# Kernel tuning notes

Measured on AMD Instinct MI355X. Metric: run time of the kernel, lower is better.

The kernel has to match this reference:

```python
import jax, jax.numpy as jnp
import numpy as np

B, S, D = 8, 1024, 1024
H, DK = 16, 64  # heads, key_size (== head_size)
NEG = 1e12


def setup_inputs() -> dict:
    key = jax.random.key(0)
    ks = jax.random.split(key, 10)
    s = 1.0 / np.sqrt(D)
    return {
        "q": jax.random.normal(ks[0], (B, S, D), jnp.float32),
        "k": jax.random.normal(ks[1], (B, S, D), jnp.float32),
        "v": jax.random.normal(ks[2], (B, S, D), jnp.float32),
        "pos_bias": jax.random.normal(ks[3], (S, S, DK), jnp.float32) * 0.02,
        "Wq": jax.random.normal(ks[4], (D, H * DK), jnp.float32) * s,
        "Wk": jax.random.normal(ks[5], (D, H * DK), jnp.float32) * s,
        "Wv": jax.random.normal(ks[6], (D, H * DK), jnp.float32) * s,
        "Wo": jax.random.normal(ks[7], (H * DK, D), jnp.float32) * s,
        "bq": jnp.zeros((H * DK,), jnp.float32),
        "bk": jnp.zeros((H * DK,), jnp.float32),
        "bv": jnp.zeros((H * DK,), jnp.float32),
        "bo": jnp.zeros((D,), jnp.float32),
        "q_mask": jnp.ones((B, S), jnp.int32),
        "v_mask": jnp.ones((B, S), jnp.int32),
    }


def reference(q, k, v, pos_bias, Wq, Wk, Wv, Wo, bq, bk, bv, bo, q_mask, v_mask):
    qm = q_mask.astype(q.dtype)  # [B,Sq]
    vm = v_mask.astype(q.dtype)  # [B,Sk]
    # Projections (faithful quirk: K is projected from v, as in the source)
    qw = (q @ Wq + bq).reshape(B, S, H, DK)
    kw = (v @ Wk + bk).reshape(B, S, H, DK)
    vw = (v @ Wv + bv).reshape(B, S, H, DK)
    # scores + inline relative-position bias ('typial_relative' branch)
    a = jnp.einsum('bjhd,bkhd->bhjk', qw, kw)
    a = a + jnp.einsum('bjhd,jkd->bhjk', qw, pos_bias)
    a = a / jnp.sqrt(jnp.asarray(DK, a.dtype))
    # additive key mask, then softmax over keys
    a = a - (1.0 - vm)[:, None, None, :] * NEG
    a = jax.nn.softmax(a, axis=-1)
    o = jnp.einsum('bhjk,bkhd->bjhd', a, vw)  # [B,Sq,H,DK]
    o = o.reshape(B, S, H * DK) @ Wo + bo
    # multiplicative query mask on output
    o = o * qm[:, :, None]
    return o
```

## Files before the change

kernel.cpp:

```cpp
#include <hip/hip_runtime.h>

using short8 = __attribute__((ext_vector_type(8))) short;
using f32x4  = __attribute__((ext_vector_type(4))) float;
using f32x16 = __attribute__((ext_vector_type(16))) float;
using u16x4  = __attribute__((ext_vector_type(4))) unsigned short;
using fl4    = __attribute__((ext_vector_type(4))) float;

#define MFMA16(a, b, c) __builtin_amdgcn_mfma_f32_16x16x32_bf16((a), (b), (c), 0, 0, 0)
#define MFMA32(a, b, c) __builtin_amdgcn_mfma_f32_32x32x16_bf16((a), (b), (c), 0, 0, 0)

static __device__ __forceinline__ unsigned short f2bf(float f) {
  union { float f; unsigned u; } x; x.f = f;
  return (unsigned short)((x.u + 0x7FFFu + ((x.u >> 16) & 1u)) >> 16);
}
static __device__ __forceinline__ float bf2f(unsigned short s) {
  union { unsigned u; float f; } x; x.u = ((unsigned)s) << 16;
  return x.f;
}
static __device__ __forceinline__ float fexp2(float x) {
  float r; asm("v_exp_f32 %0, %1" : "=v"(r) : "v"(x)); return r;
}
static __device__ __forceinline__ unsigned pk2(float lo, float hi) {
  unsigned r; asm("v_cvt_pk_bf16_f32 %0, %1, %2" : "=v"(r) : "v"(lo), "v"(hi));
  return r;
}

static __device__ __forceinline__ void gload16(const void* g, void* l) {
  __builtin_amdgcn_global_load_lds((const __attribute__((address_space(1))) void*)g,
                                   (__attribute__((address_space(3))) void*)l, 16, 0, 0);
}

#define LOG2E 1.4426950408889634f

__global__ __launch_bounds__(256) void k_wconv4(
    const float* __restrict__ W0, const float* __restrict__ W1,
    const float* __restrict__ W2, const float* __restrict__ W3,
    unsigned short* __restrict__ Wt0, unsigned short* __restrict__ Wt1,
    unsigned short* __restrict__ Wt2, unsigned short* __restrict__ Wt3) {
  const float* W = (blockIdx.z == 0) ? W0 : (blockIdx.z == 1) ? W1
                   : (blockIdx.z == 2) ? W2 : W3;
  unsigned short* Wt = (blockIdx.z == 0) ? Wt0 : (blockIdx.z == 1) ? Wt1
                       : (blockIdx.z == 2) ? Wt2 : Wt3;
  __shared__ float tile[64][65];
  const int t = threadIdx.x;
  const int n0 = blockIdx.x * 64, k0 = blockIdx.y * 64;
#pragma unroll
  for (int p = 0; p < 4; ++p) {
    int row = p * 16 + (t >> 4);
    int c4 = (t & 15) * 4;
    fl4 val = *(const fl4*)&W[(size_t)(k0 + row) * 1024 + n0 + c4];
    tile[row][c4 + 0] = val[0];
    tile[row][c4 + 1] = val[1];
    tile[row][c4 + 2] = val[2];
    tile[row][c4 + 3] = val[3];
  }
  __syncthreads();
#pragma unroll
  for (int p = 0; p < 4; ++p) {
    int n = p * 16 + (t >> 4);
    int k4 = (t & 15) * 4;
    u16x4 u;
    u[0] = f2bf(tile[k4 + 0][n]);
    u[1] = f2bf(tile[k4 + 1][n]);
    u[2] = f2bf(tile[k4 + 2][n]);
    u[3] = f2bf(tile[k4 + 3][n]);
    *(u16x4*)&Wt[(size_t)(n0 + n) * 1024 + k0 + k4] = u;
  }
}

__global__ __launch_bounds__(256) void k_cvt(const float* __restrict__ a,
                                             const float* __restrict__ b,
                                             unsigned short* __restrict__ oa,
                                             unsigned short* __restrict__ ob) {
  const float* src = blockIdx.y ? b : a;
  unsigned short* dst = blockIdx.y ? ob : oa;
  size_t i = ((size_t)blockIdx.x * 256 + threadIdx.x) * 8;
  fl4 v0 = *(const fl4*)&src[i];
  fl4 v1 = *(const fl4*)&src[i + 4];
  u16x4 u0, u1;
  u0[0] = f2bf(v0[0]); u0[1] = f2bf(v0[1]); u0[2] = f2bf(v0[2]); u0[3] = f2bf(v0[3]);
  u1[0] = f2bf(v1[0]); u1[1] = f2bf(v1[1]); u1[2] = f2bf(v1[2]); u1[3] = f2bf(v1[3]);
  *(u16x4*)&dst[i] = u0;
  *(u16x4*)&dst[i + 4] = u1;
}

#define GEMM3_CORE(APTR, BPTR)                                                  \
  const int t = threadIdx.x, lane = t & 63, w = t >> 6;                         \
  const int g = lane >> 4, ln = lane & 15;                                      \
  const int wm = w >> 1, wn = w & 1;                                            \
  __shared__ unsigned short sh[24576];    \
  const int srow = lane >> 2;                                                   \
  const int sc = (lane & 3) ^ ((lane >> 3) & 3);                                \
  const int rsw = ((ln >> 1) & 3);                                              \
  f32x4 acc[4][4] = {};                                                         \
  _Pragma("unroll") for (int pre = 0; pre < 2; ++pre) {                         \
    _Pragma("unroll") for (int p = 0; p < 2; ++p) {                             \
      gload16(&APTR[(size_t)(m0 + p * 64 + w * 16 + srow) * 1024 + pre * 32 + sc * 8], \
              &sh[pre * 8192 + (p * 64 + w * 16) * 32]);                        \
      gload16(&BPTR[(size_t)(n0 + p * 64 + w * 16 + srow) * 1024 + pre * 32 + sc * 8], \
              &sh[pre * 8192 + 4096 + (p * 64 + w * 16) * 32]);                 \
    }                                                                           \
  }                                                                             \
  int cur = 0;                                                                  \
  for (int tt = 0; tt < 32; ++tt) {                                             \
    if (tt < 31) {                                                              \
      asm volatile("s_waitcnt vmcnt(4)" ::: "memory");                          \
    } else {                                                                    \
      asm volatile("s_waitcnt vmcnt(0)" ::: "memory");                          \
    }                                                                           \
    __builtin_amdgcn_sched_barrier(0);                                          \
    __builtin_amdgcn_s_barrier();                                               \
    __builtin_amdgcn_sched_barrier(0);                                          \
    if (tt < 30) {                                                              \
      int bb = cur + 2; if (bb >= 3) bb -= 3;                                   \
      int kk = (tt + 2) * 32;                                                   \
      _Pragma("unroll") for (int p = 0; p < 2; ++p) {                           \
        gload16(&APTR[(size_t)(m0 + p * 64 + w * 16 + srow) * 1024 + kk + sc * 8], \
                &sh[bb * 8192 + (p * 64 + w * 16) * 32]);                       \
        gload16(&BPTR[(size_t)(n0 + p * 64 + w * 16 + srow) * 1024 + kk + sc * 8], \
                &sh[bb * 8192 + 4096 + (p * 64 + w * 16) * 32]);                \
      }                                                                         \
    }                                                                           \
    const unsigned short* As = &sh[cur * 8192];                                 \
    const unsigned short* Bs = As + 4096;                                       \
    short8 af[4], bfr[4];                                                       \
    _Pragma("unroll") for (int fm = 0; fm < 4; ++fm)                            \
        af[fm] = *(const short8*)&As[(wm * 64 + fm * 16 + ln) * 32 + (g ^ rsw) * 8]; \
    _Pragma("unroll") for (int fn = 0; fn < 4; ++fn)                            \
        bfr[fn] = *(const short8*)&Bs[(wn * 64 + fn * 16 + ln) * 32 + (g ^ rsw) * 8]; \
    _Pragma("unroll") for (int fn = 0; fn < 4; ++fn) {                          \
      _Pragma("unroll") for (int fm = 0; fm < 4; ++fm)                          \
          acc[fm][fn] = MFMA16(af[fm], bfr[fn], acc[fm][fn]);                   \
    }                                                                           \
    cur = (cur == 2) ? 0 : cur + 1;                                             \
  }

__global__ __launch_bounds__(256) void k_proj3(
    const unsigned short* __restrict__ QB, const unsigned short* __restrict__ VB,
    const unsigned short* __restrict__ WtQ, const unsigned short* __restrict__ WtK,
    const unsigned short* __restrict__ WtV,
    const float* __restrict__ bq, const float* __restrict__ bk,
    const float* __restrict__ bv,
    unsigned short* __restrict__ QW, unsigned short* __restrict__ KW,
    unsigned short* __restrict__ VWT) {
  const int mode = blockIdx.z;
  const unsigned short* A8 = (mode == 0) ? QB : VB;
  const unsigned short* Wt = (mode == 0) ? WtQ : (mode == 1) ? WtK : WtV;
  const float* bias = (mode == 0) ? bq : (mode == 1) ? bk : bv;
  const int m0 = blockIdx.x * 128, n0 = blockIdx.y * 128;
  GEMM3_CORE(A8, Wt)
  __syncthreads();
  const float scale = (mode == 0) ? (0.125f * LOG2E) : 1.0f;
#pragma unroll
  for (int fn = 0; fn < 4; ++fn) {
    float bn = bias[n0 + wn * 64 + fn * 16 + ln];
#pragma unroll
    for (int fm = 0; fm < 4; ++fm) {
#pragma unroll
      for (int r = 0; r < 4; ++r) {
        float val = (acc[fm][fn][r] + bn) * scale;
        sh[(wm * 64 + fm * 16 + 4 * g + r) * 132 + wn * 64 + fn * 16 + ln] = f2bf(val);
      }
    }
  }
  __syncthreads();
  if (mode < 2) {
    unsigned short* OUT = (mode == 0) ? QW : KW;
#pragma unroll
    for (int p = 0; p < 16; ++p) {
      int row = p * 8 + (t >> 5), c4 = (t & 31) * 4;
      *(u16x4*)&OUT[(size_t)(m0 + row) * 1024 + n0 + c4] =
          *(const u16x4*)&sh[row * 132 + c4];
    }
  } else {
    const int b = m0 >> 10, s0 = m0 & 1023;
#pragma unroll
    for (int p = 0; p < 16; ++p) {
#pragma unroll
      for (int qh = 0; qh < 2; ++qh) {
        int hdl = p * 8 + (t >> 5);
        int sl = qh * 64 + (t & 31) * 2;
        unsigned lo = sh[sl * 132 + hdl];
        unsigned hi = sh[(sl + 1) * 132 + hdl];
        int hd = n0 + hdl;
        int h = hd >> 6, d = hd & 63;
        *(unsigned*)&VWT[((size_t)(b * 16 + h) * 64 + d) * 1024 + s0 + sl] =
            lo | (hi << 16);
      }
    }
  }
}

__global__ __launch_bounds__(256) void k_out3(
    const unsigned short* __restrict__ OB, const unsigned short* __restrict__ WtO,
    const float* __restrict__ bo, const int* __restrict__ qmask,
    float* __restrict__ out) {
  const int m0 = blockIdx.x * 128, n0 = blockIdx.y * 128;
  GEMM3_CORE(OB, WtO)
  float bn[4];
#pragma unroll
  for (int fn = 0; fn < 4; ++fn) bn[fn] = bo[n0 + wn * 64 + fn * 16 + ln];
#pragma unroll
  for (int fm = 0; fm < 4; ++fm) {
#pragma unroll
    for (int r = 0; r < 4; ++r) {
      int row = m0 + wm * 64 + fm * 16 + 4 * g + r;
      float qm = (float)qmask[row];
#pragma unroll
      for (int fn = 0; fn < 4; ++fn)
        out[(size_t)row * 1024 + n0 + wn * 64 + fn * 16 + ln] =
            (acc[fm][fn][r] + bn[fn]) * qm;
    }
  }
}

__global__ __launch_bounds__(256) void k_pbias(
    const unsigned short* __restrict__ QW, const float* __restrict__ pb,
    const int* __restrict__ vmask, unsigned short* __restrict__ CB, int jbase) {
  const int kt = blockIdx.y;
  const int jl = blockIdx.x;
  const int j = jbase + jl;
  const int t = threadIdx.x, lane = t & 63, w = t >> 6;
  const int g = lane >> 4, ln = lane & 15;
  const int wm = w >> 1, wn = w & 1;
  __shared__ unsigned short sm[18432];
  unsigned short* a_lds = sm;
  unsigned short* b_lds = sm + 9216;
#pragma unroll
  for (int p = 0; p < 8; ++p) {
    int i4 = p * 256 + t;
    int row = i4 >> 4, c4 = (i4 & 15) * 4;
    *(u16x4*)&a_lds[row * 72 + c4] =
        *(const u16x4*)&QW[((size_t)(row >> 4) * 1024 + j) * 1024 + (row & 15) * 64 + c4];
  }
#pragma unroll
  for (int p = 0; p < 8; ++p) {
    int i4 = p * 256 + t;
    int row = i4 >> 4, c4 = (i4 & 15) * 4;
    fl4 val = *(const fl4*)&pb[((size_t)j * 1024 + kt * 128 + row) * 64 + c4];
    u16x4 u;
    u[0] = f2bf(val[0]); u[1] = f2bf(val[1]);
    u[2] = f2bf(val[2]); u[3] = f2bf(val[3]);
    *(u16x4*)&b_lds[row * 72 + c4] = u;
  }
  __syncthreads();
  f32x4 acc[4][4] = {};
#pragma unroll
  for (int ks = 0; ks < 2; ++ks) {
    short8 af[4];
#pragma unroll
    for (int fm = 0; fm < 4; ++fm)
      af[fm] = *(const short8*)&a_lds[(wm * 64 + fm * 16 + ln) * 72 + ks * 32 + 8 * g];
#pragma unroll
    for (int fn = 0; fn < 4; ++fn) {
      short8 bfr = *(const short8*)&b_lds[(wn * 64 + fn * 16 + ln) * 72 + ks * 32 + 8 * g];
#pragma unroll
      for (int fm = 0; fm < 4; ++fm) acc[fm][fn] = MFMA16(af[fm], bfr, acc[fm][fn]);
    }
  }
  __syncthreads();
#pragma unroll
  for (int fn = 0; fn < 4; ++fn) {
    int kcol = kt * 128 + wn * 64 + fn * 16 + ln;
#pragma unroll
    for (int fm = 0; fm < 4; ++fm) {
      float off = vmask[(wm * 4 + fm) * 1024 + kcol] ? 0.f : (-1e12f * LOG2E);
#pragma unroll
      for (int r = 0; r < 4; ++r)
        sm[(wm * 64 + fm * 16 + 4 * g + r) * 132 + wn * 64 + fn * 16 + ln] =
            f2bf(acc[fm][fn][r] + off);
    }
  }
  __syncthreads();
#pragma unroll
  for (int p = 0; p < 16; ++p) {
    int row = p * 8 + (t >> 5), c4 = (t & 31) * 4;
    *(u16x4*)&CB[((size_t)row * 512 + jl) * 1024 + kt * 128 + c4] =
        *(const u16x4*)&sm[row * 132 + c4];
  }
}

__global__ __launch_bounds__(256) void k_attn(
    const unsigned short* __restrict__ QW, const unsigned short* __restrict__ KW,
    const unsigned short* __restrict__ VWT, const unsigned short* __restrict__ CB,
    unsigned short* __restrict__ OB, int jbase) {
  const int B = blockIdx.x;
  const int wrk = (B & 7) * 64 + (B >> 3);
  const int jt = wrk & 3, h = (wrk >> 2) & 15, b = wrk >> 6;
  const int t = threadIdx.x, lane = t & 63, w = t >> 6;
  const int l31 = lane & 31, hf = lane >> 5;
  const int j0 = jbase + jt * 128 + w * 32;
  const int jl0 = jt * 128 + w * 32;
  __shared__ unsigned short lds_kv[2][8192];
  short8 qf[4];
  {
    const size_t qrow = ((size_t)b * 1024 + (j0 + l31)) * 1024 + h * 64;
#pragma unroll
    for (int ds = 0; ds < 4; ++ds)
      qf[ds] = *(const short8*)&QW[qrow + ds * 16 + 8 * hf];
  }
  const size_t cb_row = ((size_t)(b * 16 + h) * 512 + jl0 + l31) * 1024;

  const int src_row = w * 8 + (lane >> 3);
  const int sc = (lane & 7) ^ ((lane >> 3) & 7);
  const int rk8 = l31 & 7;

#define STAGE(kt_, bi)                                                            \
  {                                                                               \
    _Pragma("unroll") for (int r = 0; r < 2; ++r) {                               \
      gload16(&KW[((size_t)b * 1024 + (kt_) * 64 + r * 32 + src_row) * 1024 +     \
                  h * 64 + sc * 8],                                               \
              &lds_kv[bi][r * 2048 + w * 512 + lane * 8]);                        \
      gload16(&VWT[(((size_t)(b * 16 + h)) * 64 + r * 32 + src_row) * 1024 +      \
                   (kt_) * 64 + sc * 8],                                          \
              &lds_kv[bi][4096 + r * 2048 + w * 512 + lane * 8]);                 \
    }                                                                             \
  }

  u16x4 rcb[8];
#define LOAD_CB(kt_)                                                              \
  {                                                                               \
    _Pragma("unroll") for (int kf = 0; kf < 2; ++kf) {                            \
      _Pragma("unroll") for (int q = 0; q < 4; ++q)                               \
          rcb[kf * 4 + q] = *(const u16x4*)&CB[cb_row + (kt_) * 64 + kf * 32 +    \
                                               q * 8 + 4 * hf];                   \
    }                                                                             \
  }

  STAGE(0, 0);
  __builtin_amdgcn_sched_barrier(0);
  LOAD_CB(0);
  __builtin_amdgcn_sched_barrier(0);
  STAGE(1, 1);
  __builtin_amdgcn_sched_barrier(0);

  f32x16 o_acc[2] = {};
  float l_par = 0.f;

  for (int kt = 0; kt < 16; ++kt) {
    if (kt == 0) {
      asm volatile("s_waitcnt vmcnt(12)" ::: "memory");
    } else {
      asm volatile("s_waitcnt vmcnt(8)" ::: "memory");
    }
    __builtin_amdgcn_sched_barrier(0);
    __builtin_amdgcn_s_barrier();
    __builtin_amdgcn_sched_barrier(0);
    if (kt >= 1 && kt < 15) STAGE(kt + 1, (kt + 1) & 1);
    __builtin_amdgcn_sched_barrier(0);
    f32x16 st[2];
#pragma unroll
    for (int kf = 0; kf < 2; ++kf) {
#pragma unroll
      for (int q = 0; q < 4; ++q) {
#pragma unroll
        for (int r = 0; r < 4; ++r) st[kf][q * 4 + r] = bf2f(rcb[kf * 4 + q][r]);
      }
    }
    if (kt < 15) LOAD_CB(kt + 1);
    __builtin_amdgcn_sched_barrier(0);
    const unsigned short* Kb = lds_kv[kt & 1];
    const unsigned short* Vb = Kb + 4096;
    __builtin_amdgcn_s_setprio(1);
#pragma unroll
    for (int ds = 0; ds < 4; ++ds) {
#pragma unroll
      for (int kf = 0; kf < 2; ++kf) {
        short8 af =
            *(const short8*)&Kb[(kf * 32 + l31) * 64 + (((ds * 2 + hf) ^ rk8) * 8)];
        st[kf] = MFMA32(af, qf[ds], st[kf]);
      }
    }
    __builtin_amdgcn_s_setprio(0);
#pragma unroll
    for (int ks = 0; ks < 4; ++ks) {
      const int kf = ks >> 1, bs = (ks & 1) * 8;
      float e0 = fexp2(st[kf][bs + 0] - 17.0f), e1 = fexp2(st[kf][bs + 1] - 17.0f);
      float e2 = fexp2(st[kf][bs + 2] - 17.0f), e3 = fexp2(st[kf][bs + 3] - 17.0f);
      float e4 = fexp2(st[kf][bs + 4] - 17.0f), e5 = fexp2(st[kf][bs + 5] - 17.0f);
      float e6 = fexp2(st[kf][bs + 6] - 17.0f), e7 = fexp2(st[kf][bs + 7] - 17.0f);
      l_par += ((e0 + e1) + (e2 + e3)) + ((e4 + e5) + (e6 + e7));
      unsigned A0 = pk2(e0, e1), A1 = pk2(e2, e3);
      unsigned C0 = pk2(e4, e5), C1 = pk2(e6, e7);
      asm("v_permlane32_swap_b32 %0, %1" : "+v"(A0), "+v"(C0));
      asm("v_permlane32_swap_b32 %0, %1" : "+v"(A1), "+v"(C1));
      union { short8 v; unsigned u[4]; } bp;
      bp.u[0] = A0; bp.u[1] = A1; bp.u[2] = C0; bp.u[3] = C1;
      __builtin_amdgcn_s_setprio(1);
#pragma unroll
      for (int df = 0; df < 2; ++df) {
        short8 av = *(const short8*)&Vb[(df * 32 + l31) * 64 +
                                        (((ks * 2 + hf) ^ rk8) * 8)];
        o_acc[df] = MFMA32(av, bp.v, o_acc[df]);
      }
      __builtin_amdgcn_s_setprio(0);
    }
  }
  l_par += __shfl_xor(l_par, 32);
  float inv = 1.0f / l_par;
  const size_t orow = ((size_t)b * 1024 + (j0 + l31)) * 1024 + h * 64;
#pragma unroll
  for (int df = 0; df < 2; ++df) {
#pragma unroll
    for (int q = 0; q < 4; ++q) {
      union { u16x4 v; unsigned u[2]; } uo;
      uo.u[0] = pk2(o_acc[df][q * 4 + 0] * inv, o_acc[df][q * 4 + 1] * inv);
      uo.u[1] = pk2(o_acc[df][q * 4 + 2] * inv, o_acc[df][q * 4 + 3] * inv);
      *(u16x4*)&OB[orow + df * 32 + q * 8 + 4 * hf] = uo.v;
    }
  }
#undef STAGE
#undef LOAD_CB
}

extern "C" void kernel_launch(void* const* d_in, const int* in_sizes, int n_in,
                              void* d_out, int out_size, void* d_ws, size_t ws_size,
                              hipStream_t stream) {
  const float* q  = (const float*)d_in[0];
  const float* v  = (const float*)d_in[2];
  const float* pb = (const float*)d_in[3];
  const float* Wq = (const float*)d_in[4];
  const float* Wk = (const float*)d_in[5];
  const float* Wv = (const float*)d_in[6];
  const float* Wo = (const float*)d_in[7];
  const float* bq = (const float*)d_in[8];
  const float* bk = (const float*)d_in[9];
  const float* bv = (const float*)d_in[10];
  const float* bo = (const float*)d_in[11];
  const int* qm = (const int*)d_in[12];
  const int* vm = (const int*)d_in[13];
  float* out = (float*)d_out;

  unsigned short* ws = (unsigned short*)d_ws;
  const size_t M1 = 1024 * 1024;
  unsigned short* WTQ = ws;
  unsigned short* WTK = WTQ + M1;
  unsigned short* WTV = WTK + M1;
  unsigned short* WTO = WTV + M1;
  unsigned short* QB  = WTO + M1;
  unsigned short* VB  = QB + 8 * M1;
  unsigned short* QW  = VB + 8 * M1;
  unsigned short* KW  = QW + 8 * M1;
  unsigned short* VWT = KW + 8 * M1;
  unsigned short* OB  = VWT + 8 * M1;
  unsigned short* CB  = OB + 8 * M1;

  k_wconv4<<<dim3(16, 16, 4), 256, 0, stream>>>(Wq, Wk, Wv, Wo, WTQ, WTK, WTV, WTO);
  k_cvt<<<dim3(4096, 2), 256, 0, stream>>>(q, v, QB, VB);
  k_proj3<<<dim3(64, 8, 3), 256, 0, stream>>>(QB, VB, WTQ, WTK, WTV, bq, bk, bv,
                                              QW, KW, VWT);
  for (int st = 0; st < 2; ++st) {
    k_pbias<<<dim3(512, 8), 256, 0, stream>>>(QW, pb, vm, CB, st * 512);
    k_attn<<<dim3(512), 256, 0, stream>>>(QW, KW, VWT, CB, OB, st * 512);
  }
  k_out3<<<dim3(64, 8), 256, 0, stream>>>(OB, WTO, bo, qm, out);
}
```

Before: 339.5 us.

## Merge prep kernels and fuse K/V projections sharing the A tile

Merges the weight transpose/convert kernel and the q/v bf16 conversion kernel into a single launch. Splits the combined projection kernel into a Q projection and a fused K+V projection, where each block loads a V-input tile once and multiplies it against both Wk and Wv, halving A-operand traffic for those GEMMs. The KV kernel uses more LDS (72KB) and twice the accumulator registers, which may reduce occupancy, and it issues half as many blocks as the two separate GEMMs did.

Result: no change. 346.2 us (+2.0%).

```diff
diff --git a/kernel.cpp b/kernel.cpp
--- a/kernel.cpp
+++ b/kernel.cpp
@@ -32,128 +32,124 @@
 
 #define LOG2E 1.4426950408889634f
 
-__global__ __launch_bounds__(256) void k_wconv4(
+__global__ __launch_bounds__(256) void k_prep(
     const float* __restrict__ W0, const float* __restrict__ W1,
     const float* __restrict__ W2, const float* __restrict__ W3,
     unsigned short* __restrict__ Wt0, unsigned short* __restrict__ Wt1,
-    unsigned short* __restrict__ Wt2, unsigned short* __restrict__ Wt3) {
-  const float* W = (blockIdx.z == 0) ? W0 : (blockIdx.z == 1) ? W1
-                   : (blockIdx.z == 2) ? W2 : W3;
-  unsigned short* Wt = (blockIdx.z == 0) ? Wt0 : (blockIdx.z == 1) ? Wt1
-                       : (blockIdx.z == 2) ? Wt2 : Wt3;
+    unsigned short* __restrict__ Wt2, unsigned short* __restrict__ Wt3,
+    const float* __restrict__ qf, const float* __restrict__ vf,
+    unsigned short* __restrict__ QB, unsigned short* __restrict__ VB) {
   __shared__ float tile[64][65];
+  const int bx = blockIdx.x;
   const int t = threadIdx.x;
-  const int n0 = blockIdx.x * 64, k0 = blockIdx.y * 64;
-#pragma unroll
-  for (int p = 0; p < 4; ++p) {
-    int row = p * 16 + (t >> 4);
-    int c4 = (t & 15) * 4;
-    fl4 val = *(const fl4*)&W[(size_t)(k0 + row) * 1024 + n0 + c4];
-    tile[row][c4 + 0] = val[0];
-    tile[row][c4 + 1] = val[1];
-    tile[row][c4 + 2] = val[2];
-    tile[row][c4 + 3] = val[3];
-  }
-  __syncthreads();
-#pragma unroll
-  for (int p = 0; p < 4; ++p) {
-    int n = p * 16 + (t >> 4);
-    int k4 = (t & 15) * 4;
-    u16x4 u;
-    u[0] = f2bf(tile[k4 + 0][n]);
-    u[1] = f2bf(tile[k4 + 1][n]);
-    u[2] = f2bf(tile[k4 + 2][n]);
-    u[3] = f2bf(tile[k4 + 3][n]);
-    *(u16x4*)&Wt[(size_t)(n0 + n) * 1024 + k0 + k4] = u;
-  }
-}
-
-__global__ __launch_bounds__(256) void k_cvt(const float* __restrict__ a,
-                                             const float* __restrict__ b,
-                                             unsigned short* __restrict__ oa,
-                                             unsigned short* __restrict__ ob) {
-  const float* src = blockIdx.y ? b : a;
-  unsigned short* dst = blockIdx.y ? ob : oa;
-  size_t i = ((size_t)blockIdx.x * 256 + threadIdx.x) * 8;
-  fl4 v0 = *(const fl4*)&src[i];
-  fl4 v1 = *(const fl4*)&src[i + 4];
-  u16x4 u0, u1;
-  u0[0] = f2bf(v0[0]); u0[1] = f2bf(v0[1]); u0[2] = f2bf(v0[2]); u0[3] = f2bf(v0[3]);
-  u1[0] = f2bf(v1[0]); u1[1] = f2bf(v1[1]); u1[2] = f2bf(v1[2]); u1[3] = f2bf(v1[3]);
-  *(u16x4*)&dst[i] = u0;
-  *(u16x4*)&dst[i + 4] = u1;
-}
-
-#define GEMM3_CORE(APTR, BPTR)                                                  \
-  const int t = threadIdx.x, lane = t & 63, w = t >> 6;                         \
-  const int g = lane >> 4, ln = lane & 15;                                      \
-  const int wm = w >> 1, wn = w & 1;                                            \
-  __shared__ unsigned short sh[24576];    \
-  const int srow = lane >> 2;                                                   \
-  const int sc = (lane & 3) ^ ((lane >> 3) & 3);                                \
-  const int rsw = ((ln >> 1) & 3);                                              \
-  f32x4 acc[4][4] = {};                                                         \
-  _Pragma("unroll") for (int pre = 0; pre < 2; ++pre) {                         \
-    _Pragma("unroll") for (int p = 0; p < 2; ++p) {                             \
-      gload16(&APTR[(size_t)(m0 + p * 64 + w * 16 + srow) * 1024 + pre * 32 + sc * 8], \
-              &sh[pre * 8192 + (p * 64 + w * 16) * 32]);                        \
-      gload16(&BPTR[(size_t)(n0 + p * 64 + w * 16 + srow) * 1024 + pre * 32 + sc * 8], \
-              &sh[pre * 8192 + 4096 + (p * 64 + w * 16) * 32]);                 \
-    }                                                                           \
-  }                                                                             \
-  int cur = 0;                                                                  \
-  for (int tt = 0; tt < 32; ++tt) {                                             \
-    if (tt < 31) {                                                              \
-      asm volatile("s_waitcnt vmcnt(4)" ::: "memory");                          \
-    } else {                                                                    \
-      asm volatile("s_waitcnt vmcnt(0)" ::: "memory");                          \
-    }                                                                           \
-    __builtin_amdgcn_sched_barrier(0);                                          \
-    __builtin_amdgcn_s_barrier();                                               \
-    __builtin_amdgcn_sched_barrier(0);                                          \
-    if (tt < 30) {                                                              \
-      int bb = cur + 2; if (bb >= 3) bb -= 3;                                   \
-      int kk = (tt + 2) * 32;                                                   \
-      _Pragma("unroll") for (int p = 0; p < 2; ++p) {                           \
-        gload16(&APTR[(size_t)(m0 + p * 64 + w * 16 + srow) * 1024 + kk + sc * 8], \
-                &sh[bb * 8192 + (p * 64 + w * 16) * 32]);                       \
-        gload16(&BPTR[(size_t)(n0 + p * 64 + w * 16 + srow) * 1024 + kk + sc * 8], \
-                &sh[bb * 8192 + 4096 + (p * 64 + w * 16) * 32]);                \
-      }                                                                         \
-    }                                                                           \
-    const unsigned short* As = &sh[cur * 8192];                                 \
-    const unsigned short* Bs = As + 4096;                                       \
-    short8 af[4], bfr[4];                                                       \
-    _Pragma("unroll") for (int fm = 0; fm < 4; ++fm)                            \
-        af[fm] = *(const short8*)&As[(wm * 64 + fm * 16 + ln) * 32 + (g ^ rsw) * 8]; \
-    _Pragma("unroll") for (int fn = 0; fn < 4; ++fn)                            \
-        bfr[fn] = *(const short8*)&Bs[(wn * 64 + fn * 16 + ln) * 32 + (g ^ rsw) * 8]; \
-    _Pragma("unroll") for (int fn = 0; fn < 4; ++fn) {                          \
-      _Pragma("unroll") for (int fm = 0; fm < 4; ++fm)                          \
-          acc[fm][fn] = MFMA16(af[fm], bfr[fn], acc[fm][fn]);                   \
-    }                                                                           \
-    cur = (cur == 2) ? 0 : cur + 1;                                             \
-  }
-
-__global__ __launch_bounds__(256) void k_proj3(
-    const unsigned short* __restrict__ QB, const unsigned short* __restrict__ VB,
-    const unsigned short* __restrict__ WtQ, const unsigned short* __restrict__ WtK,
-    const unsigned short* __restrict__ WtV,
-    const float* __restrict__ bq, const float* __restrict__ bk,
-    const float* __restrict__ bv,
-    unsigned short* __restrict__ QW, unsigned short* __restrict__ KW,
-    unsigned short* __restrict__ VWT) {
-  const int mode = blockIdx.z;
-  const unsigned short* A8 = (mode == 0) ? QB : VB;
-  const unsigned short* Wt = (mode == 0) ? WtQ : (mode == 1) ? WtK : WtV;
-  const float* bias = (mode == 0) ? bq : (mode == 1) ? bk : bv;
+  if (bx < 1024) {
+    const int z = bx >> 8, yy = (bx >> 4) & 15, xx = bx & 15;
+    const float* W = (z == 0) ? W0 : (z == 1) ? W1 : (z == 2) ? W2 : W3;
+    unsigned short* Wt = (z == 0) ? Wt0 : (z == 1) ? Wt1 : (z == 2) ? Wt2 : Wt3;
+    const int n0 = xx * 64, k0 = yy * 64;
+#pragma unroll
+    for (int p = 0; p < 4; ++p) {
+      int row = p * 16 + (t >> 4);
+      int c4 = (t & 15) * 4;
+      fl4 val = *(const fl4*)&W[(size_t)(k0 + row) * 1024 + n0 + c4];
+      tile[row][c4 + 0] = val[0];
+      tile[row][c4 + 1] = val[1];
+      tile[row][c4 + 2] = val[2];
+      tile[row][c4 + 3] = val[3];
+    }
+    __syncthreads();
+#pragma unroll
+    for (int p = 0; p < 4; ++p) {
+      int n = p * 16 + (t >> 4);
+      int k4 = (t & 15) * 4;
+      u16x4 u;
+      u[0] = f2bf(tile[k4 + 0][n]);
+      u[1] = f2bf(tile[k4 + 1][n]);
+      u[2] = f2bf(tile[k4 + 2][n]);
+      u[3] = f2bf(tile[k4 + 3][n]);
+      *(u16x4*)&Wt[(size_t)(n0 + n) * 1024 + k0 + k4] = u;
+    }
+  } else {
+    const int idx = bx - 1024;
+    const int half = idx >> 12;
+    const int blk = idx & 4095;
+    const float* src = half ? vf : qf;
+    unsigned short* dst = half ? VB : QB;
+    size_t i = ((size_t)blk * 256 + t) * 8;
+    fl4 v0 = *(const fl4*)&src[i];
+    fl4 v1 = *(const fl4*)&src[i + 4];
+    u16x4 u0, u1;
+    u0[0] = f2bf(v0[0]); u0[1] = f2bf(v0[1]); u0[2] = f2bf(v0[2]); u0[3] = f2bf(v0[3]);
+    u1[0] = f2bf(v1[0]); u1[1] = f2bf(v1[1]); u1[2] = f2bf(v1[2]); u1[3] = f2bf(v1[3]);
+    *(u16x4*)&dst[i] = u0;
+    *(u16x4*)&dst[i + 4] = u1;
+  }
+}
+
+__global__ __launch_bounds__(256) void k_projQ(
+    const unsigned short* __restrict__ QB, const unsigned short* __restrict__ WtQ,
+    const float* __restrict__ bq, unsigned short* __restrict__ QW) {
   const int m0 = blockIdx.x * 128, n0 = blockIdx.y * 128;
-  GEMM3_CORE(A8, Wt)
-  __syncthreads();
-  const float scale = (mode == 0) ? (0.125f * LOG2E) : 1.0f;
+  const int t = threadIdx.x, lane = t & 63, w = t >> 6;
+  const int g = lane >> 4, ln = lane & 15;
+  const int wm = w >> 1, wn = w & 1;
+  __shared__ unsigned short sh[24576];
+  const int srow = lane >> 2;
+  const int sc = (lane & 3) ^ ((lane >> 3) & 3);
+  const int rsw = ((ln >> 1) & 3);
+  f32x4 acc[4][4] = {};
+#pragma unroll
+  for (int pre = 0; pre < 2; ++pre) {
+#pragma unroll
+    for (int p = 0; p < 2; ++p) {
+      gload16(&QB[(size_t)(m0 + p * 64 + w * 16 + srow) * 1024 + pre * 32 + sc * 8],
+              &sh[pre * 8192 + (p * 64 + w * 16) * 32]);
+      gload16(&WtQ[(size_t)(n0 + p * 64 + w * 16 + srow) * 1024 + pre * 32 + sc * 8],
+              &sh[pre * 8192 + 4096 + (p * 64 + w * 16) * 32]);
+    }
+  }
+  int cur = 0;
+  for (int tt = 0; tt < 32; ++tt) {
+    if (tt < 31) {
+      asm volatile("s_waitcnt vmcnt(4)" ::: "memory");
+    } else {
+      asm volatile("s_waitcnt vmcnt(0)" ::: "memory");
+    }
+    __builtin_amdgcn_sched_barrier(0);
+    __builtin_amdgcn_s_barrier();
+    __builtin_amdgcn_sched_barrier(0);
+    if (tt < 30) {
+      int bb = cur + 2; if (bb >= 3) bb -= 3;
+      int kk = (tt + 2) * 32;
+#pragma unroll
+      for (int p = 0; p < 2; ++p) {
+        gload16(&QB[(size_t)(m0 + p * 64 + w * 16 + srow) * 1024 + kk + sc * 8],
+                &sh[bb * 8192 + (p * 64 + w * 16) * 32]);
+        gload16(&WtQ[(size_t)(n0 + p * 64 + w * 16 + srow) * 1024 + kk + sc * 8],
+                &sh[bb * 8192 + 4096 + (p * 64 + w * 16) * 32]);
+      }
+    }
+    const unsigned short* As = &sh[cur * 8192];
+    const unsigned short* Bs = As + 4096;
+    short8 af[4], bfr[4];
+#pragma unroll
+    for (int fm = 0; fm < 4; ++fm)
+      af[fm] = *(const short8*)&As[(wm * 64 + fm * 16 + ln) * 32 + (g ^ rsw) * 8];
+#pragma unroll
+    for (int fn = 0; fn < 4; ++fn)
+      bfr[fn] = *(const short8*)&Bs[(wn * 64 + fn * 16 + ln) * 32 + (g ^ rsw) * 8];
+#pragma unroll
+    for (int fn = 0; fn < 4; ++fn) {
+#pragma unroll
+      for (int fm = 0; fm < 4; ++fm) acc[fm][fn] = MFMA16(af[fm], bfr[fn], acc[fm][fn]);
+    }
+    cur = (cur == 2) ? 0 : cur + 1;
+  }
+  __syncthreads();
+  const float scale = 0.125f * LOG2E;
 #pragma unroll
   for (int fn = 0; fn < 4; ++fn) {
-    float bn = bias[n0 + wn * 64 + fn * 16 + ln];
+    float bn = bq[n0 + wn * 64 + fn * 16 + ln];
 #pragma unroll
     for (int fm = 0; fm < 4; ++fm) {
 #pragma unroll
@@ -164,15 +160,118 @@
     }
   }
   __syncthreads();
-  if (mode < 2) {
-    unsigned short* OUT = (mode == 0) ? QW : KW;
-#pragma unroll
-    for (int p = 0; p < 16; ++p) {
-      int row = p * 8 + (t >> 5), c4 = (t & 31) * 4;
-      *(u16x4*)&OUT[(size_t)(m0 + row) * 1024 + n0 + c4] =
-          *(const u16x4*)&sh[row * 132 + c4];
-    }
-  } else {
+#pragma unroll
+  for (int p = 0; p < 16; ++p) {
+    int row = p * 8 + (t >> 5), c4 = (t & 31) * 4;
+    *(u16x4*)&QW[(size_t)(m0 + row) * 1024 + n0 + c4] =
+        *(const u16x4*)&sh[row * 132 + c4];
+  }
+}
+
+__global__ __launch_bounds__(256) void k_projKV(
+    const unsigned short* __restrict__ VB, const unsigned short* __restrict__ WtK,
+    const unsigned short* __restrict__ WtV, const float* __restrict__ bk,
+    const float* __restrict__ bv, unsigned short* __restrict__ KW,
+    unsigned short* __restrict__ VWT) {
+  const int m0 = blockIdx.x * 128, n0 = blockIdx.y * 128;
+  const int t = threadIdx.x, lane = t & 63, w = t >> 6;
+  const int g = lane >> 4, ln = lane & 15;
+  const int wm = w >> 1, wn = w & 1;
+  __shared__ unsigned short sh[36864];
+  const int srow = lane >> 2;
+  const int sc = (lane & 3) ^ ((lane >> 3) & 3);
+  const int rsw = ((ln >> 1) & 3);
+  f32x4 accK[4][4] = {}, accV[4][4] = {};
+#pragma unroll
+  for (int pre = 0; pre < 2; ++pre) {
+#pragma unroll
+    for (int p = 0; p < 2; ++p) {
+      gload16(&VB[(size_t)(m0 + p * 64 + w * 16 + srow) * 1024 + pre * 32 + sc * 8],
+              &sh[pre * 12288 + (p * 64 + w * 16) * 32]);
+      gload16(&WtK[(size_t)(n0 + p * 64 + w * 16 + srow) * 1024 + pre * 32 + sc * 8],
+              &sh[pre * 12288 + 4096 + (p * 64 + w * 16) * 32]);
+      gload16(&WtV[(size_t)(n0 + p * 64 + w * 16 + srow) * 1024 + pre * 32 + sc * 8],
+              &sh[pre * 12288 + 8192 + (p * 64 + w * 16) * 32]);
+    }
+  }
+  int cur = 0;
+  for (int tt = 0; tt < 32; ++tt) {
+    if (tt < 31) {
+      asm volatile("s_waitcnt vmcnt(6)" ::: "memory");
+    } else {
+      asm volatile("s_waitcnt vmcnt(0)" ::: "memory");
+    }
+    __builtin_amdgcn_sched_barrier(0);
+    __builtin_amdgcn_s_barrier();
+    __builtin_amdgcn_sched_barrier(0);
+    if (tt < 30) {
+      int bb = cur + 2; if (bb >= 3) bb -= 3;
+      int kk = (tt + 2) * 32;
+#pragma unroll
+      for (int p = 0; p < 2; ++p) {
+        gload16(&VB[(size_t)(m0 + p * 64 + w * 16 + srow) * 1024 + kk + sc * 8],
+                &sh[bb * 12288 + (p * 64 + w * 16) * 32]);
+        gload16(&WtK[(size_t)(n0 + p * 64 + w * 16 + srow) * 1024 + kk + sc * 8],
+                &sh[bb * 12288 + 4096 + (p * 64 + w * 16) * 32]);
+        gload16(&WtV[(size_t)(n0 + p * 64 + w * 16 + srow) * 1024 + kk + sc * 8],
+                &sh[bb * 12288 + 8192 + (p * 64 + w * 16) * 32]);
+      }
+    }
+    const unsigned short* As = &sh[cur * 12288];
+    const unsigned short* BKs = As + 4096;
+    const unsigned short* BVs = As + 8192;
+    short8 af[4], bk8[4], bv8[4];
+#pragma unroll
+    for (int fm = 0; fm < 4; ++fm)
+      af[fm] = *(const short8*)&As[(wm * 64 + fm * 16 + ln) * 32 + (g ^ rsw) * 8];
+#pragma unroll
+    for (int fn = 0; fn < 4; ++fn) {
+      bk8[fn] = *(const short8*)&BKs[(wn * 64 + fn * 16 + ln) * 32 + (g ^ rsw) * 8];
+      bv8[fn] = *(const short8*)&BVs[(wn * 64 + fn * 16 + ln) * 32 + (g ^ rsw) * 8];
+    }
+#pragma unroll
+    for (int fn = 0; fn < 4; ++fn) {
+#pragma unroll
+      for (int fm = 0; fm < 4; ++fm) {
+        accK[fm][fn] = MFMA16(af[fm], bk8[fn], accK[fm][fn]);
+        accV[fm][fn] = MFMA16(af[fm], bv8[fn], accV[fm][fn]);
+      }
+    }
+    cur = (cur == 2) ? 0 : cur + 1;
+  }
+  __syncthreads();
+#pragma unroll
+  for (int fn = 0; fn < 4; ++fn) {
+    float bn = bk[n0 + wn * 64 + fn * 16 + ln];
+#pragma unroll
+    for (int fm = 0; fm < 4; ++fm) {
+#pragma unroll
+      for (int r = 0; r < 4; ++r)
+        sh[(wm * 64 + fm * 16 + 4 * g + r) * 132 + wn * 64 + fn * 16 + ln] =
+            f2bf(accK[fm][fn][r] + bn);
+    }
+  }
+  __syncthreads();
+#pragma unroll
+  for (int p = 0; p < 16; ++p) {
+    int row = p * 8 + (t >> 5), c4 = (t & 31) * 4;
+    *(u16x4*)&KW[(size_t)(m0 + row) * 1024 + n0 + c4] =
+        *(const u16x4*)&sh[row * 132 + c4];
+  }
+  __syncthreads();
+#pragma unroll
+  for (int fn = 0; fn < 4; ++fn) {
+    float bn = bv[n0 + wn * 64 + fn * 16 + ln];
+#pragma unroll
+    for (int fm = 0; fm < 4; ++fm) {
+#pragma unroll
+      for (int r = 0; r < 4; ++r)
+        sh[(wm * 64 + fm * 16 + 4 * g + r) * 132 + wn * 64 + fn * 16 + ln] =
+            f2bf(accV[fm][fn][r] + bn);
+    }
+  }
+  __syncthreads();
+  {
     const int b = m0 >> 10, s0 = m0 & 1023;
 #pragma unroll
     for (int p = 0; p < 16; ++p) {
@@ -196,7 +295,61 @@
     const float* __restrict__ bo, const int* __restrict__ qmask,
     float* __restrict__ out) {
   const int m0 = blockIdx.x * 128, n0 = blockIdx.y * 128;
-  GEMM3_CORE(OB, WtO)
+  const int t = threadIdx.x, lane = t & 63, w = t >> 6;
+  const int g = lane >> 4, ln = lane & 15;
+  const int wm = w >> 1, wn = w & 1;
+  __shared__ unsigned short sh[24576];
+  const int srow = lane >> 2;
+  const int sc = (lane & 3) ^ ((lane >> 3) & 3);
+  const int rsw = ((ln >> 1) & 3);
+  f32x4 acc[4][4] = {};
+#pragma unroll
+  for (int pre = 0; pre < 2; ++pre) {
+#pragma unroll
+    for (int p = 0; p < 2; ++p) {
+      gload16(&OB[(size_t)(m0 + p * 64 + w * 16 + srow) * 1024 + pre * 32 + sc * 8],
+              &sh[pre * 8192 + (p * 64 + w * 16) * 32]);
+      gload16(&WtO[(size_t)(n0 + p * 64 + w * 16 + srow) * 1024 + pre * 32 + sc * 8],
+              &sh[pre * 8192 + 4096 + (p * 64 + w * 16) * 32]);
+    }
+  }
+  int cur = 0;
+  for (int tt = 0; tt < 32; ++tt) {
+    if (tt < 31) {
+      asm volatile("s_waitcnt vmcnt(4)" ::: "memory");
+    } else {
+      asm volatile("s_waitcnt vmcnt(0)" ::: "memory");
+    }
+    __builtin_amdgcn_sched_barrier(0);
+    __builtin_amdgcn_s_barrier();
+    __builtin_amdgcn_sched_barrier(0);
+    if (tt < 30) {
+      int bb = cur + 2; if (bb >= 3) bb -= 3;
+      int kk = (tt + 2) * 32;
+#pragma unroll
+      for (int p = 0; p < 2; ++p) {
+        gload16(&OB[(size_t)(m0 + p * 64 + w * 16 + srow) * 1024 + kk + sc * 8],
+                &sh[bb * 8192 + (p * 64 + w * 16) * 32]);
+        gload16(&WtO[(size_t)(n0 + p * 64 + w * 16 + srow) * 1024 + kk + sc * 8],
+                &sh[bb * 8192 + 4096 + (p * 64 + w * 16) * 32]);
+      }
+    }
+    const unsigned short* As = &sh[cur * 8192];
+    const unsigned short* Bs = As + 4096;
+    short8 af[4], bfr[4];
+#pragma unroll
+    for (int fm = 0; fm < 4; ++fm)
+      af[fm] = *(const short8*)&As[(wm * 64 + fm * 16 + ln) * 32 + (g ^ rsw) * 8];
+#pragma unroll
+    for (int fn = 0; fn < 4; ++fn)
+      bfr[fn] = *(const short8*)&Bs[(wn * 64 + fn * 16 + ln) * 32 + (g ^ rsw) * 8];
+#pragma unroll
+    for (int fn = 0; fn < 4; ++fn) {
+#pragma unroll
+      for (int fm = 0; fm < 4; ++fm) acc[fm][fn] = MFMA16(af[fm], bfr[fn], acc[fm][fn]);
+    }
+    cur = (cur == 2) ? 0 : cur + 1;
+  }
   float bn[4];
 #pragma unroll
   for (int fn = 0; fn < 4; ++fn) bn[fn] = bo[n0 + wn * 64 + fn * 16 + ln];
@@ -445,10 +598,10 @@
   unsigned short* OB  = VWT + 8 * M1;
   unsigned short* CB  = OB + 8 * M1;
 
-  k_wconv4<<<dim3(16, 16, 4), 256, 0, stream>>>(Wq, Wk, Wv, Wo, WTQ, WTK, WTV, WTO);
-  k_cvt<<<dim3(4096, 2), 256, 0, stream>>>(q, v, QB, VB);
-  k_proj3<<<dim3(64, 8, 3), 256, 0, stream>>>(QB, VB, WTQ, WTK, WTV, bq, bk, bv,
-                                              QW, KW, VWT);
+  k_prep<<<dim3(9216), 256, 0, stream>>>(Wq, Wk, Wv, Wo, WTQ, WTK, WTV, WTO,
+                                         q, v, QB, VB);
+  k_projQ<<<dim3(64, 8), 256, 0, stream>>>(QB, WTQ, bq, QW);
+  k_projKV<<<dim3(64, 8), 256, 0, stream>>>(VB, WTK, WTV, bk, bv, KW, VWT);
   for (int st = 0; st < 2; ++st) {
     k_pbias<<<dim3(512, 8), 256, 0, stream>>>(QW, pb, vm, CB, st * 512);
     k_attn<<<dim3(512), 256, 0, stream>>>(QW, KW, VWT, CB, OB, st * 512);
```
